# Kernel tuning notes

Hardware: AMD Instinct MI355X
Metric: run time of the kernel (lower is better)

The kernel has to match this reference:

```python
import jax, jax.numpy as jnp
import numpy as np

NEG_BIG = -9e15
ALPHA = 0.2  # LeakyReLU negative slope


def _gatm_layer(x, adj_mask, M, W, a_self, a_neighs):
    # x: [N, Fin], adj_mask: [N, N] bool, M: [N, N]
    h = x @ W                                   # [N, Fout]
    s = h @ a_self                              # [N, 1]
    n = h @ a_neighs                            # [N, 1]
    e = s + n.T                                 # [N, N] broadcast additive score
    e = jax.nn.leaky_relu(e * M, negative_slope=ALPHA)
    scores = jnp.where(adj_mask, e, NEG_BIG)
    attention = jax.nn.softmax(scores, axis=1)  # row-wise
    h_prime = attention @ h                     # [N, Fout]
    return jax.nn.elu(h_prime)                  # concat=True path


def setup_inputs() -> dict:
    key = jax.random.key(0)
    ks = jax.random.split(key, 8)
    N, D0, D1, D2 = 8192, 512, 256, 64
    scale = 0.05
    return {
        "x": jax.random.normal(ks[0], (N, D0), dtype=jnp.float32),
        "adj": jax.random.randint(ks[1], (N, N), 0, 2, dtype=jnp.int32),
        "M": jax.random.uniform(ks[2], (N, N), dtype=jnp.float32),
        "W0": jax.random.normal(ks[3], (D0, D1), dtype=jnp.float32) * scale,
        "a_self0": jax.random.normal(ks[4], (D1, 1), dtype=jnp.float32) * scale,
        "a_neighs0": jax.random.normal(ks[5], (D1, 1), dtype=jnp.float32) * scale,
        "W1": jax.random.normal(ks[6], (D1, D2), dtype=jnp.float32) * scale,
        "a_self1": jax.random.normal(ks[7], (D2, 1), dtype=jnp.float32) * scale,
        "a_neighs1": jax.random.normal(jax.random.fold_in(key, 99), (D2, 1), dtype=jnp.float32) * scale,
    }


def reference(x, adj, M, W0, a_self0, a_neighs0, W1, a_self1, a_neighs1):
    adj_mask = adj > 0
    x = _gatm_layer(x, adj_mask, M, W0, a_self0, a_neighs0)
    x = _gatm_layer(x, adj_mask, M, W1, a_self1, a_neighs1)
    return x
```

## Files before the change

kernel.cpp:

```cpp
#include <hip/hip_runtime.h>
#include <hip/hip_bf16.h>

constexpr int NN = 8192;
using uint = unsigned int;

typedef __bf16 bf16x8 __attribute__((ext_vector_type(8)));
typedef float f32x4 __attribute__((ext_vector_type(4)));
typedef float f32x16 __attribute__((ext_vector_type(16)));
typedef unsigned short ushort8_t __attribute__((ext_vector_type(8)));

__device__ __forceinline__ float eluf(float z) { return z > 0.f ? z : __expf(z) - 1.f; }

__device__ __forceinline__ unsigned short bf16_hi(float v) {
  unsigned u = __float_as_uint(v);
  unsigned r = u + 0x7fffu + ((u >> 16) & 1u);
  return (unsigned short)(r >> 16);
}
__device__ __forceinline__ float bf16_tof(unsigned short u) {
  return __uint_as_float(((unsigned)u) << 16);
}

__device__ __forceinline__ uint cvt_pk_bf16(float a, float b) {
  uint r;
  asm("v_cvt_pk_bf16_f32 %0, %1, %2" : "=v"(r) : "v"(a), "v"(b));
  return r;
}

__device__ __forceinline__ void lds_barrier() {
  asm volatile("s_waitcnt lgkmcnt(0)" ::: "memory");
  __builtin_amdgcn_s_barrier();
}

template<int K, int NOUT>
__global__ __launch_bounds__(256) void gemm_kernel(
    const float* __restrict__ A, const float* __restrict__ W, float* __restrict__ C) {
  constexpr int BM = 64, BN = 64, BK = 16;
  __shared__ __align__(16) float As[BK][BM + 4];
  __shared__ __align__(16) float Ws[BK][BN];
  const int t = threadIdx.x;
  const int i0 = blockIdx.x * BM;
  const int c0 = blockIdx.y * BN;
  const int tr = t >> 4;
  const int tc = t & 15;
  const int lr = t >> 2;
  const int lk = (t & 3) * 4;
  const int wk = t >> 4;
  const int wc = (t & 15) * 4;
  float acc[4][4] = {};
  for (int k0 = 0; k0 < K; k0 += BK) {
    const float4 a4 = *reinterpret_cast<const float4*>(&A[(size_t)(i0 + lr) * K + k0 + lk]);
    As[lk + 0][lr] = a4.x; As[lk + 1][lr] = a4.y;
    As[lk + 2][lr] = a4.z; As[lk + 3][lr] = a4.w;
    *reinterpret_cast<float4*>(&Ws[wk][wc]) =
        *reinterpret_cast<const float4*>(&W[(size_t)(k0 + wk) * NOUT + c0 + wc]);
    __syncthreads();
    #pragma unroll
    for (int kk = 0; kk < BK; ++kk) {
      const float4 av = *reinterpret_cast<const float4*>(&As[kk][4 * tr]);
      const float4 wv = *reinterpret_cast<const float4*>(&Ws[kk][4 * tc]);
      const float a[4] = {av.x, av.y, av.z, av.w};
      const float w[4] = {wv.x, wv.y, wv.z, wv.w};
      #pragma unroll
      for (int i = 0; i < 4; ++i)
        #pragma unroll
        for (int j = 0; j < 4; ++j) acc[i][j] += a[i] * w[j];
    }
    __syncthreads();
  }
  #pragma unroll
  for (int i = 0; i < 4; ++i) {
    const float4 o = make_float4(acc[i][0], acc[i][1], acc[i][2], acc[i][3]);
    *reinterpret_cast<float4*>(&C[(size_t)(i0 + 4 * tr + i) * NOUT + c0 + 4 * tc]) = o;
  }
}

__global__ __launch_bounds__(256) void splitx_kernel(
    const float* __restrict__ X, unsigned short* __restrict__ Th,
    unsigned short* __restrict__ Tl) {
  const size_t tid = (size_t)blockIdx.x * 256 + threadIdx.x;
  const int kt = (int)(tid >> 13);
  const int row = (int)(tid & 8191);
  const float* src = X + (size_t)row * 512 + kt * 32;
  #pragma unroll
  for (int kc = 0; kc < 4; ++kc) {
    ushort8_t hi, lo;
    #pragma unroll
    for (int e = 0; e < 8; ++e) {
      const float v = src[kc * 8 + e];
      const unsigned short h = bf16_hi(v);
      hi[e] = h;
      lo[e] = bf16_hi(v - bf16_tof(h));
    }
    const size_t o = ((size_t)(kt * 4 + kc) * 8192 + row) * 8;
    *reinterpret_cast<ushort8_t*>(&Th[o]) = hi;
    *reinterpret_cast<ushort8_t*>(&Tl[o]) = lo;
  }
}

__global__ __launch_bounds__(256) void splitw_kernel(
    const float* __restrict__ W, unsigned short* __restrict__ Th,
    unsigned short* __restrict__ Tl) {
  const int tid = blockIdx.x * 256 + threadIdx.x;
  const int kb = tid >> 8;
  const int col = tid & 255;
  ushort8_t hi, lo;
  #pragma unroll
  for (int e = 0; e < 8; ++e) {
    const float v = W[(size_t)(kb * 8 + e) * 256 + col];
    const unsigned short h = bf16_hi(v);
    hi[e] = h;
    lo[e] = bf16_hi(v - bf16_tof(h));
  }
  const size_t o = ((size_t)kb * 256 + col) * 8;
  *reinterpret_cast<ushort8_t*>(&Th[o]) = hi;
  *reinterpret_cast<ushort8_t*>(&Tl[o]) = lo;
}

__global__ __launch_bounds__(512) void gemm1_mfma_kernel(
    const unsigned short* __restrict__ Axh, const unsigned short* __restrict__ Axl,
    const unsigned short* __restrict__ Bwh, const unsigned short* __restrict__ Bwl,
    float* __restrict__ C) {
  const int t = threadIdx.x;
  const int lane = t & 63;
  const int cf = t >> 6;
  const int i0 = blockIdx.x * 32;
  const int col = cf * 32 + (lane & 31);
  const size_t abase = ((size_t)(lane >> 5) * 8192 + i0 + (lane & 31)) * 8;
  const size_t bbase = ((size_t)(lane >> 5) * 256 + col) * 8;

  f32x16 acc;
  #pragma unroll
  for (int i = 0; i < 16; ++i) acc[i] = 0.f;

  #pragma unroll 2
  for (int kt = 0; kt < 16; ++kt) {
    const size_t at = (size_t)kt * 4 * 8192 * 8;
    const size_t bt = (size_t)kt * 4 * 256 * 8;
    #pragma unroll
    for (int h = 0; h < 2; ++h) {
      const size_t ao = at + (size_t)h * 2 * 8192 * 8 + abase;
      const size_t bo = bt + (size_t)h * 2 * 256 * 8 + bbase;
      const bf16x8 ah = *reinterpret_cast<const bf16x8*>(Axh + ao);
      const bf16x8 al = *reinterpret_cast<const bf16x8*>(Axl + ao);
      const bf16x8 bh = *reinterpret_cast<const bf16x8*>(Bwh + bo);
      const bf16x8 bl = *reinterpret_cast<const bf16x8*>(Bwl + bo);
      acc = __builtin_amdgcn_mfma_f32_32x32x16_bf16(al, bh, acc, 0, 0, 0);
      acc = __builtin_amdgcn_mfma_f32_32x32x16_bf16(ah, bl, acc, 0, 0, 0);
      acc = __builtin_amdgcn_mfma_f32_32x32x16_bf16(ah, bh, acc, 0, 0, 0);
    }
  }

  #pragma unroll
  for (int reg = 0; reg < 16; ++reg) {
    const int row = (reg & 3) + 8 * (reg >> 2) + 4 * (lane >> 5);
    C[(size_t)(i0 + row) * 256 + col] = acc[reg];
  }
}

template<int FOUT>
__global__ __launch_bounds__(256) void sn_kernel(
    const float* __restrict__ H, const float* __restrict__ a_self,
    const float* __restrict__ a_neigh, float* __restrict__ s, float* __restrict__ n) {
  const int wave = threadIdx.x >> 6;
  const int lane = threadIdx.x & 63;
  const int row = blockIdx.x * 4 + wave;
  float ds = 0.f, dn = 0.f;
  #pragma unroll
  for (int c = lane; c < FOUT; c += 64) {
    const float h = H[(size_t)row * FOUT + c];
    ds += h * a_self[c];
    dn += h * a_neigh[c];
  }
  #pragma unroll
  for (int off = 32; off > 0; off >>= 1) {
    ds += __shfl_down(ds, off);
    dn += __shfl_down(dn, off);
  }
  if (lane == 0) { s[row] = ds; n[row] = dn; }
}

template<int F>
__global__ __launch_bounds__(256) void split_kernel(
    const float* __restrict__ H, unsigned short* __restrict__ Th,
    unsigned short* __restrict__ Tl) {
  const int t = threadIdx.x;
  const int tile = blockIdx.x;
  const int c = t & (F - 1);
  const int kcb = t / F;
  for (int kc = kcb; kc < 4; kc += 256 / F) {
    ushort8_t hi, lo;
    #pragma unroll
    for (int e = 0; e < 8; ++e) {
      float v = H[(size_t)(tile * 32 + kc * 8 + e) * F + c];
      unsigned short h = bf16_hi(v);
      hi[e] = h;
      lo[e] = bf16_hi(v - bf16_tof(h));
    }
    size_t o = ((size_t)(tile * 4 + kc) * F + c) * 8;
    *reinterpret_cast<ushort8_t*>(&Th[o]) = hi;
    *reinterpret_cast<ushort8_t*>(&Tl[o]) = lo;
  }
}

__global__ __launch_bounds__(256) void mask_kernel(
    const int* __restrict__ adj, uint* __restrict__ Bm) {
  const size_t tg = (size_t)blockIdx.x * 256 + threadIdx.x;
  const int4 a = *reinterpret_cast<const int4*>(&adj[tg * 4]);
  uint nib = (a.x > 0 ? 1u : 0u) | (a.y > 0 ? 2u : 0u) |
             (a.z > 0 ? 4u : 0u) | (a.w > 0 ? 8u : 0u);
  const int lane = threadIdx.x & 63;
  uint v = nib << ((lane & 7) * 4);
  v |= __shfl_xor(v, 1);
  v |= __shfl_xor(v, 2);
  v |= __shfl_xor(v, 4);
  if ((lane & 7) == 0) Bm[tg >> 3] = v;
}

template<int F>
__global__ __launch_bounds__(256) void combine_kernel(
    const float* __restrict__ pO, const float* __restrict__ pL, float* __restrict__ out) {
  const size_t q = (size_t)blockIdx.x * 256 + threadIdx.x;
  const size_t base = q * 4;
  const int row = (int)(base / F);
  const float4 a = *reinterpret_cast<const float4*>(pO + base);
  const float4 b = *reinterpret_cast<const float4*>(pO + (size_t)8192 * F + base);
  const float il = 1.0f / (pL[row] + pL[8192 + row]);
  float4 o;
  o.x = eluf((a.x + b.x) * il);
  o.y = eluf((a.y + b.y) * il);
  o.z = eluf((a.z + b.z) * il);
  o.w = eluf((a.w + b.w) * il);
  *reinterpret_cast<float4*>(out + base) = o;
}

__global__ __launch_bounds__(1024, 4) void attn1_kernel(
    const float* __restrict__ Mm, const uint* __restrict__ Bm,
    const float* __restrict__ sv, const float* __restrict__ nv,
    const unsigned short* __restrict__ Th, const unsigned short* __restrict__ Tl,
    float* __restrict__ pO, float* __restrict__ pL) {
  constexpr int F = 256, NT = 4096 / 64;
  __shared__ __align__(16) uint Pa[2][2][2][8 * 132];
  __shared__ __align__(16) float nvs[8192];
  __shared__ float l_lds[64];

  const int t = threadIdx.x;
  const int lane = t & 63;
  const int w = t >> 6;
  const int cf = w & 7;
  const int ks = w >> 3;
  const int r = t >> 5;
  const int p2 = t & 31;
  const int i0 = blockIdx.x * 64;
  const int jh = blockIdx.y;
  const size_t jbase = (size_t)jh * 4096;
  const int jt = jh * 128;

  reinterpret_cast<float4*>(nvs)[t] = reinterpret_cast<const float4*>(nv + jbase)[t];

  const float svrA = sv[i0 + r];
  const float svrB = sv[i0 + 32 + r];
  const size_t mrowA = (size_t)(i0 + r) * NN + jbase;
  const size_t mrowB = mrowA + (size_t)32 * NN;
  const uint* mkrowA = Bm + (size_t)(i0 + r) * (NN / 32) + jh * 128;
  const uint* mkrowB = mkrowA + (size_t)32 * (NN / 32);
  const int col = cf * 32 + (lane & 31);
  const size_t bo0 = ((size_t)(lane >> 5) * F + col) * 8;
  const int pidx = (p2 >> 2) * 132 + r * 4 + (p2 & 3);
  const int aidx = (ks * 4 + (lane >> 5)) * 132 + (lane & 31) * 4;

  float2 MA_e = *reinterpret_cast<const float2*>(&Mm[mrowA + 2 * p2]);
  float2 MA_o = *reinterpret_cast<const float2*>(&Mm[mrowA + 64 + 2 * p2]);
  float2 MB_e = *reinterpret_cast<const float2*>(&Mm[mrowB + 2 * p2]);
  float2 MB_o = *reinterpret_cast<const float2*>(&Mm[mrowB + 64 + 2 * p2]);
  uint mkA_e = mkrowA[p2 >> 4];
  uint mkA_o = mkrowA[2 + (p2 >> 4)];
  uint mkB_e = mkrowB[p2 >> 4];
  uint mkB_o = mkrowB[2 + (p2 >> 4)];
  const size_t tb0 = (size_t)(jt + ks) * 8192;
  bf16x8 bh0_e = *reinterpret_cast<const bf16x8*>(Th + tb0 + bo0);
  bf16x8 bl0_e = *reinterpret_cast<const bf16x8*>(Tl + tb0 + bo0);
  bf16x8 bh1_e = *reinterpret_cast<const bf16x8*>(Th + tb0 + bo0 + 4096);
  bf16x8 bl1_e = *reinterpret_cast<const bf16x8*>(Tl + tb0 + bo0 + 4096);
  bf16x8 bh0_o, bl0_o, bh1_o, bl1_o;

  float rsumA = 0.f, rsumB = 0.f;
  f32x16 accA, accB;
  #pragma unroll
  for (int i = 0; i < 16; ++i) { accA[i] = 0.f; accB[i] = 0.f; }

  __syncthreads();

  float2 nv_e = *reinterpret_cast<const float2*>(&nvs[2 * p2]);
  float2 nv_o = *reinterpret_cast<const float2*>(&nvs[64 + 2 * p2]);

#define STEP1(TJ, MCA, MKA, MCB, MKB, NVC, BH0C, BL0C, BH1C, BL1C, BH0N, BL0N, BH1N, BL1N) \
  {                                                                               \
    const int t_j = (TJ);                                                         \
    const int jb = (t_j + 1 < NT) ? t_j + 1 : 0;                                  \
    const size_t tb = (size_t)(jt + 2 * jb + ks) * 8192;                          \
    BH0N = *reinterpret_cast<const bf16x8*>(Th + tb + bo0);                       \
    BL0N = *reinterpret_cast<const bf16x8*>(Tl + tb + bo0);                       \
    BH1N = *reinterpret_cast<const bf16x8*>(Th + tb + bo0 + 4096);                \
    BL1N = *reinterpret_cast<const bf16x8*>(Tl + tb + bo0 + 4096);                \
    float e0 = (svrA + NVC.x) * MCA.x; e0 = fmaxf(e0, 0.2f * e0); e0 = fminf(e0, 70.f); \
    float e1 = (svrA + NVC.y) * MCA.y; e1 = fmaxf(e1, 0.2f * e1); e1 = fminf(e1, 70.f); \
    float e2 = (svrB + NVC.x) * MCB.x; e2 = fmaxf(e2, 0.2f * e2); e2 = fminf(e2, 70.f); \
    float e3 = (svrB + NVC.y) * MCB.y; e3 = fmaxf(e3, 0.2f * e3); e3 = fminf(e3, 70.f); \
    const float pA0 = ((MKA >> (2 * (p2 & 15))) & 1u) ? __expf(e0) : 0.f;         \
    const float pA1 = ((MKA >> (2 * (p2 & 15) + 1)) & 1u) ? __expf(e1) : 0.f;     \
    const float pB0 = ((MKB >> (2 * (p2 & 15))) & 1u) ? __expf(e2) : 0.f;         \
    const float pB1 = ((MKB >> (2 * (p2 & 15) + 1)) & 1u) ? __expf(e3) : 0.f;     \
    rsumA += pA0 + pA1; rsumB += pB0 + pB1;                                       \
    const int jm = (t_j + 2 < NT) ? t_j + 2 : 0;                                  \
    MCA = *reinterpret_cast<const float2*>(&Mm[mrowA + (size_t)jm * 64 + 2 * p2]); \
    MKA = mkrowA[jm * 2 + (p2 >> 4)];                                             \
    MCB = *reinterpret_cast<const float2*>(&Mm[mrowB + (size_t)jm * 64 + 2 * p2]); \
    MKB = mkrowB[jm * 2 + (p2 >> 4)];                                             \
    NVC = *reinterpret_cast<const float2*>(&nvs[jm * 64 + 2 * p2]);               \
    const uint hwA = cvt_pk_bf16(pA0, pA1);                                       \
    const uint lwA = cvt_pk_bf16(pA0 - __uint_as_float(hwA << 16),                \
                                 pA1 - __uint_as_float(hwA & 0xffff0000u));       \
    const uint hwB = cvt_pk_bf16(pB0, pB1);                                       \
    const uint lwB = cvt_pk_bf16(pB0 - __uint_as_float(hwB << 16),                \
                                 pB1 - __uint_as_float(hwB & 0xffff0000u));       \
    Pa[t_j & 1][0][0][pidx] = hwA;                                                \
    Pa[t_j & 1][1][0][pidx] = lwA;                                                \
    Pa[t_j & 1][0][1][pidx] = hwB;                                                \
    Pa[t_j & 1][1][1][pidx] = lwB;                                                \
    lds_barrier();                                                                \
    const bf16x8 ahA0 = *reinterpret_cast<const bf16x8*>(&Pa[t_j & 1][0][0][aidx]);       \
    const bf16x8 alA0 = *reinterpret_cast<const bf16x8*>(&Pa[t_j & 1][1][0][aidx]);       \
    const bf16x8 ahA1 = *reinterpret_cast<const bf16x8*>(&Pa[t_j & 1][0][0][aidx + 264]); \
    const bf16x8 alA1 = *reinterpret_cast<const bf16x8*>(&Pa[t_j & 1][1][0][aidx + 264]); \
    const bf16x8 ahB0 = *reinterpret_cast<const bf16x8*>(&Pa[t_j & 1][0][1][aidx]);       \
    const bf16x8 alB0 = *reinterpret_cast<const bf16x8*>(&Pa[t_j & 1][1][1][aidx]);       \
    const bf16x8 ahB1 = *reinterpret_cast<const bf16x8*>(&Pa[t_j & 1][0][1][aidx + 264]); \
    const bf16x8 alB1 = *reinterpret_cast<const bf16x8*>(&Pa[t_j & 1][1][1][aidx + 264]); \
    accA = __builtin_amdgcn_mfma_f32_32x32x16_bf16(alA0, BH0C, accA, 0, 0, 0);    \
    accB = __builtin_amdgcn_mfma_f32_32x32x16_bf16(alB0, BH0C, accB, 0, 0, 0);    \
    accA = __builtin_amdgcn_mfma_f32_32x32x16_bf16(ahA0, BL0C, accA, 0, 0, 0);    \
    accB = __builtin_amdgcn_mfma_f32_32x32x16_bf16(ahB0, BL0C, accB, 0, 0, 0);    \
    accA = __builtin_amdgcn_mfma_f32_32x32x16_bf16(ahA0, BH0C, accA, 0, 0, 0);    \
    accB = __builtin_amdgcn_mfma_f32_32x32x16_bf16(ahB0, BH0C, accB, 0, 0, 0);    \
    accA = __builtin_amdgcn_mfma_f32_32x32x16_bf16(alA1, BH1C, accA, 0, 0, 0);    \
    accB = __builtin_amdgcn_mfma_f32_32x32x16_bf16(alB1, BH1C, accB, 0, 0, 0);    \
    accA = __builtin_amdgcn_mfma_f32_32x32x16_bf16(ahA1, BL1C, accA, 0, 0, 0);    \
    accB = __builtin_amdgcn_mfma_f32_32x32x16_bf16(ahB1, BL1C, accB, 0, 0, 0);    \
    accA = __builtin_amdgcn_mfma_f32_32x32x16_bf16(ahA1, BH1C, accA, 0, 0, 0);    \
    accB = __builtin_amdgcn_mfma_f32_32x32x16_bf16(ahB1, BH1C, accB, 0, 0, 0);    \
  }

  for (int tj = 0; tj < NT; tj += 2) {
    STEP1(tj,     MA_e, mkA_e, MB_e, mkB_e, nv_e, bh0_e, bl0_e, bh1_e, bl1_e, bh0_o, bl0_o, bh1_o, bl1_o)
    STEP1(tj + 1, MA_o, mkA_o, MB_o, mkB_o, nv_o, bh0_o, bl0_o, bh1_o, bl1_o, bh0_e, bl0_e, bh1_e, bl1_e)
  }
#undef STEP1

  #pragma unroll
  for (int off = 1; off < 32; off <<= 1) {
    rsumA += __shfl_xor(rsumA, off);
    rsumB += __shfl_xor(rsumB, off);
  }
  if (p2 == 0) { l_lds[r] = rsumA; l_lds[32 + r] = rsumB; }
  __syncthreads();
  if (t < 64) pL[(size_t)jh * 8192 + i0 + t] = l_lds[t];

  float* scratch = nvs;
  if (ks == 1) {
    #pragma unroll
    for (int reg = 0; reg < 16; ++reg) scratch[cf * 1024 + reg * 64 + lane] = accA[reg];
  }
  __syncthreads();
  if (ks == 0) {
    #pragma unroll
    for (int reg = 0; reg < 16; ++reg) {
      const int row = (reg & 3) + 8 * (reg >> 2) + 4 * (lane >> 5);
      pO[(size_t)jh * 8192 * F + (size_t)(i0 + row) * F + col] =
          accA[reg] + scratch[cf * 1024 + reg * 64 + lane];
    }
  }
  __syncthreads();
  if (ks == 1) {
    #pragma unroll
    for (int reg = 0; reg < 16; ++reg) scratch[cf * 1024 + reg * 64 + lane] = accB[reg];
  }
  __syncthreads();
  if (ks == 0) {
    #pragma unroll
    for (int reg = 0; reg < 16; ++reg) {
      const int row = (reg & 3) + 8 * (reg >> 2) + 4 * (lane >> 5);
      pO[(size_t)jh * 8192 * F + (size_t)(i0 + 32 + row) * F + col] =
          accB[reg] + scratch[cf * 1024 + reg * 64 + lane];
    }
  }
}

__global__ __launch_bounds__(1024, 4) void attn2_kernel(
    const float* __restrict__ Mm, const uint* __restrict__ Bm,
    const float* __restrict__ sv, const float* __restrict__ nv,
    const unsigned short* __restrict__ Th, const unsigned short* __restrict__ Tl,
    float* __restrict__ pO, float* __restrict__ pL) {
  constexpr int F = 64, NT = 4096 / 64;
  __shared__ __align__(16) uint Pa[2][2][2][8 * 132];
  __shared__ __align__(16) float nvs[4096];
  __shared__ float l_lds[64];

  const int t = threadIdx.x;
  const int lane = t & 63;
  const int w = t >> 6;
  const int rb = w & 1;
  const int cf = (w >> 1) & 3;
  const int ks = w >> 3;
  const int r = t >> 5;
  const int p2 = t & 31;
  const int i0 = blockIdx.x * 64;
  const int jh = blockIdx.y;
  const size_t jbase = (size_t)jh * 4096;
  const int jt = jh * 128;

  reinterpret_cast<float4*>(nvs)[t] = reinterpret_cast<const float4*>(nv + jbase)[t];

  const float svrA = sv[i0 + r];
  const float svrB = sv[i0 + 32 + r];
  const size_t mrowA = (size_t)(i0 + r) * NN + jbase;
  const size_t mrowB = mrowA + (size_t)32 * NN;
  const uint* mkrowA = Bm + (size_t)(i0 + r) * (NN / 32) + jh * 128;
  const uint* mkrowB = mkrowA + (size_t)32 * (NN / 32);
  const int col = cf * 16 + (lane & 15);
  const size_t bo2 = ((size_t)(lane >> 4) * F + col) * 8;
  const int pidx = (p2 >> 2) * 132 + r * 4 + (p2 & 3);
  const int aidx = (ks * 4 + (lane >> 4)) * 132 + (rb * 16 + (lane & 15)) * 4;

  float2 MA_e = *reinterpret_cast<const float2*>(&Mm[mrowA + 2 * p2]);
  float2 MA_o = *reinterpret_cast<const float2*>(&Mm[mrowA + 64 + 2 * p2]);
  float2 MB_e = *reinterpret_cast<const float2*>(&Mm[mrowB + 2 * p2]);
  float2 MB_o = *reinterpret_cast<const float2*>(&Mm[mrowB + 64 + 2 * p2]);
  uint mkA_e = mkrowA[p2 >> 4];
  uint mkA_o = mkrowA[2 + (p2 >> 4)];
  uint mkB_e = mkrowB[p2 >> 4];
  uint mkB_o = mkrowB[2 + (p2 >> 4)];
  const size_t tb0 = (size_t)(jt + ks) * 2048;
  bf16x8 bh_e = *reinterpret_cast<const bf16x8*>(Th + tb0 + bo2);
  bf16x8 bl_e = *reinterpret_cast<const bf16x8*>(Tl + tb0 + bo2);
  bf16x8 bh_o, bl_o;

  float rsumA = 0.f, rsumB = 0.f;
  f32x4 accA = {0.f, 0.f, 0.f, 0.f}, accA2 = {0.f, 0.f, 0.f, 0.f};
  f32x4 accB = {0.f, 0.f, 0.f, 0.f}, accB2 = {0.f, 0.f, 0.f, 0.f};

  __syncthreads();

  float2 nv_e = *reinterpret_cast<const float2*>(&nvs[2 * p2]);
  float2 nv_o = *reinterpret_cast<const float2*>(&nvs[64 + 2 * p2]);

#define STEP2(TJ, MCA, MKA, MCB, MKB, NVC, BHC, BLC, BHN, BLN)                    \
  {                                                                               \
    const int t_j = (TJ);                                                         \
    const int jb = (t_j + 1 < NT) ? t_j + 1 : 0;                                  \
    const size_t tb = (size_t)(jt + 2 * jb + ks) * 2048;                          \
    BHN = *reinterpret_cast<const bf16x8*>(Th + tb + bo2);                        \
    BLN = *reinterpret_cast<const bf16x8*>(Tl + tb + bo2);                        \
    float e0 = (svrA + NVC.x) * MCA.x; e0 = fmaxf(e0, 0.2f * e0); e0 = fminf(e0, 70.f); \
    float e1 = (svrA + NVC.y) * MCA.y; e1 = fmaxf(e1, 0.2f * e1); e1 = fminf(e1, 70.f); \
    float e2 = (svrB + NVC.x) * MCB.x; e2 = fmaxf(e2, 0.2f * e2); e2 = fminf(e2, 70.f); \
    float e3 = (svrB + NVC.y) * MCB.y; e3 = fmaxf(e3, 0.2f * e3); e3 = fminf(e3, 70.f); \
    const float pA0 = ((MKA >> (2 * (p2 & 15))) & 1u) ? __expf(e0) : 0.f;         \
    const float pA1 = ((MKA >> (2 * (p2 & 15) + 1)) & 1u) ? __expf(e1) : 0.f;     \
    const float pB0 = ((MKB >> (2 * (p2 & 15))) & 1u) ? __expf(e2) : 0.f;         \
    const float pB1 = ((MKB >> (2 * (p2 & 15) + 1)) & 1u) ? __expf(e3) : 0.f;     \
    rsumA += pA0 + pA1; rsumB += pB0 + pB1;                                       \
    const int jm = (t_j + 2 < NT) ? t_j + 2 : 0;                                  \
    MCA = *reinterpret_cast<const float2*>(&Mm[mrowA + (size_t)jm * 64 + 2 * p2]); \
    MKA = mkrowA[jm * 2 + (p2 >> 4)];                                             \
    MCB = *reinterpret_cast<const float2*>(&Mm[mrowB + (size_t)jm * 64 + 2 * p2]); \
    MKB = mkrowB[jm * 2 + (p2 >> 4)];                                             \
    NVC = *reinterpret_cast<const float2*>(&nvs[jm * 64 + 2 * p2]);               \
    const uint hwA = cvt_pk_bf16(pA0, pA1);                                       \
    const uint lwA = cvt_pk_bf16(pA0 - __uint_as_float(hwA << 16),                \
                                 pA1 - __uint_as_float(hwA & 0xffff0000u));       \
    const uint hwB = cvt_pk_bf16(pB0, pB1);                                       \
    const uint lwB = cvt_pk_bf16(pB0 - __uint_as_float(hwB << 16),                \
                                 pB1 - __uint_as_float(hwB & 0xffff0000u));       \
    Pa[t_j & 1][0][0][pidx] = hwA;                                                \
    Pa[t_j & 1][1][0][pidx] = lwA;                                                \
    Pa[t_j & 1][0][1][pidx] = hwB;                                                \
    Pa[t_j & 1][1][1][pidx] = lwB;                                                \
    lds_barrier();                                                                \
    const bf16x8 ahA = *reinterpret_cast<const bf16x8*>(&Pa[t_j & 1][0][0][aidx]); \
    const bf16x8 alA = *reinterpret_cast<const bf16x8*>(&Pa[t_j & 1][1][0][aidx]); \
    const bf16x8 ahB = *reinterpret_cast<const bf16x8*>(&Pa[t_j & 1][0][1][aidx]); \
    const bf16x8 alB = *reinterpret_cast<const bf16x8*>(&Pa[t_j & 1][1][1][aidx]); \
    accA  = __builtin_amdgcn_mfma_f32_16x16x32_bf16(alA, BHC, accA, 0, 0, 0);     \
    accB  = __builtin_amdgcn_mfma_f32_16x16x32_bf16(alB, BHC, accB, 0, 0, 0);     \
    accA2 = __builtin_amdgcn_mfma_f32_16x16x32_bf16(ahA, BLC, accA2, 0, 0, 0);    \
    accB2 = __builtin_amdgcn_mfma_f32_16x16x32_bf16(ahB, BLC, accB2, 0, 0, 0);    \
    accA  = __builtin_amdgcn_mfma_f32_16x16x32_bf16(ahA, BHC, accA, 0, 0, 0);     \
    accB  = __builtin_amdgcn_mfma_f32_16x16x32_bf16(ahB, BHC, accB, 0, 0, 0);     \
  }

  for (int tj = 0; tj < NT; tj += 2) {
    STEP2(tj,     MA_e, mkA_e, MB_e, mkB_e, nv_e, bh_e, bl_e, bh_o, bl_o)
    STEP2(tj + 1, MA_o, mkA_o, MB_o, mkB_o, nv_o, bh_o, bl_o, bh_e, bl_e)
  }
#undef STEP2

  #pragma unroll
  for (int off = 1; off < 32; off <<= 1) {
    rsumA += __shfl_xor(rsumA, off);
    rsumB += __shfl_xor(rsumB, off);
  }
  if (p2 == 0) { l_lds[r] = rsumA; l_lds[32 + r] = rsumB; }
  __syncthreads();
  if (t < 64) pL[(size_t)jh * 8192 + i0 + t] = l_lds[t];

  float* scratch = nvs;
  if (ks == 1) {
    #pragma unroll
    for (int reg = 0; reg < 4; ++reg)
      scratch[(w & 7) * 256 + reg * 64 + lane] = accA[reg] + accA2[reg];
  }
  __syncthreads();
  if (ks == 0) {
    #pragma unroll
    for (int reg = 0; reg < 4; ++reg) {
      const int row = rb * 16 + (lane >> 4) * 4 + reg;
      pO[(size_t)jh * 8192 * F + (size_t)(i0 + row) * F + col] =
          accA[reg] + accA2[reg] + scratch[(w & 7) * 256 + reg * 64 + lane];
    }
  }
  __syncthreads();
  if (ks == 1) {
    #pragma unroll
    for (int reg = 0; reg < 4; ++reg)
      scratch[(w & 7) * 256 + reg * 64 + lane] = accB[reg] + accB2[reg];
  }
  __syncthreads();
  if (ks == 0) {
    #pragma unroll
    for (int reg = 0; reg < 4; ++reg) {
      const int row = rb * 16 + (lane >> 4) * 4 + reg;
      pO[(size_t)jh * 8192 * F + (size_t)(i0 + 32 + row) * F + col] =
          accB[reg] + accB2[reg] + scratch[(w & 7) * 256 + reg * 64 + lane];
    }
  }
}

extern "C" void kernel_launch(void* const* d_in, const int* in_sizes, int n_in,
                              void* d_out, int out_size, void* d_ws, size_t ws_size,
                              hipStream_t stream) {
  const float* x   = (const float*)d_in[0];
  const int*   adj = (const int*)  d_in[1];
  const float* Mm  = (const float*)d_in[2];
  const float* W0  = (const float*)d_in[3];
  const float* as0 = (const float*)d_in[4];
  const float* an0 = (const float*)d_in[5];
  const float* W1  = (const float*)d_in[6];
  const float* as1 = (const float*)d_in[7];
  const float* an1 = (const float*)d_in[8];
  float* out = (float*)d_out;

  char* ws = (char*)d_ws;
  const size_t MB = 1048576;
  const size_t KB = 1024;
  float* h0  = (float*)(ws);
  uint*  Bm  = (uint*) (ws);
  float* x1  = (float*)(ws + 8 * MB);
  float* h1  = (float*)(ws + 16 * MB);
  unsigned short* Th0 = (unsigned short*)(ws + 18 * MB);
  unsigned short* Tl0 = (unsigned short*)(ws + 22 * MB);
  unsigned short* Th1 = (unsigned short*)(ws + 26 * MB);
  unsigned short* Tl1 = (unsigned short*)(ws + 27 * MB);
  float* s0  = (float*)(ws + 28 * MB);
  float* n0  = (float*)(ws + 28 * MB + 32 * KB);
  float* s1  = (float*)(ws + 28 * MB + 64 * KB);
  float* n1  = (float*)(ws + 28 * MB + 96 * KB);
  float* pL1 = (float*)(ws + 28 * MB + 128 * KB);
  float* pL2 = (float*)(ws + 28 * MB + 192 * KB);
  float* pO1 = (float*)(ws + 29 * MB);
  float* pO2 = (float*)(ws + 29 * MB);
  unsigned short* Txh = (unsigned short*)(ws + 64 * MB);
  unsigned short* Txl = (unsigned short*)(ws + 72 * MB);
  unsigned short* Twh = (unsigned short*)(ws + 80 * MB);
  unsigned short* Twl = (unsigned short*)(ws + 81 * MB);

  splitx_kernel<<<dim3(512), dim3(256), 0, stream>>>(x, Txh, Txl);
  splitw_kernel<<<dim3(64), dim3(256), 0, stream>>>(W0, Twh, Twl);
  gemm1_mfma_kernel<<<dim3(256), dim3(512), 0, stream>>>(Txh, Txl, Twh, Twl, h0);
  sn_kernel<256><<<dim3(2048), dim3(256), 0, stream>>>(h0, as0, an0, s0, n0);
  split_kernel<256><<<dim3(256), dim3(256), 0, stream>>>(h0, Th0, Tl0);
  mask_kernel<<<dim3(65536), dim3(256), 0, stream>>>(adj, Bm);
  attn1_kernel<<<dim3(128, 2), dim3(1024), 0, stream>>>(Mm, Bm, s0, n0, Th0, Tl0, pO1, pL1);
  combine_kernel<256><<<dim3(2048), dim3(256), 0, stream>>>(pO1, pL1, x1);
  gemm_kernel<256, 64><<<dim3(128, 1), dim3(256), 0, stream>>>(x1, W1, h1);
  sn_kernel<64><<<dim3(2048), dim3(256), 0, stream>>>(h1, as1, an1, s1, n1);
  split_kernel<64><<<dim3(256), dim3(256), 0, stream>>>(h1, Th1, Tl1);
  attn2_kernel<<<dim3(128, 2), dim3(1024), 0, stream>>>(Mm, Bm, s1, n1, Th1, Tl1, pO2, pL2);
  combine_kernel<64><<<dim3(512), dim3(256), 0, stream>>>(pO2, pL2, out);
}
```

Measured before the change: 329.4 us.

## Fuse split into gemm1 epilogue and fuse combine+gemm2+sn+split for layer two

The bf16 hi/lo split of h0 now happens in the gemm1 epilogue, which removes the separate split kernel and its re-read of h0. For the second layer, the combine (normalize plus ELU) is folded into the A-tile load of the fp32 GEMM. The s/n dot products and the hi/lo split are computed in that GEMM's epilogue, which removes the x1 and h1 round trips and three launches. The costs are scattered 2-byte stores in both epilogues and an extra tiny kernel that computes the inverse row sums.

```diff
diff --git a/kernel.cpp b/kernel.cpp
--- a/kernel.cpp
+++ b/kernel.cpp
@@ -29,49 +29,6 @@
 __device__ __forceinline__ void lds_barrier() {
   asm volatile("s_waitcnt lgkmcnt(0)" ::: "memory");
   __builtin_amdgcn_s_barrier();
-}
-
-template<int K, int NOUT>
-__global__ __launch_bounds__(256) void gemm_kernel(
-    const float* __restrict__ A, const float* __restrict__ W, float* __restrict__ C) {
-  constexpr int BM = 64, BN = 64, BK = 16;
-  __shared__ __align__(16) float As[BK][BM + 4];
-  __shared__ __align__(16) float Ws[BK][BN];
-  const int t = threadIdx.x;
-  const int i0 = blockIdx.x * BM;
-  const int c0 = blockIdx.y * BN;
-  const int tr = t >> 4;
-  const int tc = t & 15;
-  const int lr = t >> 2;
-  const int lk = (t & 3) * 4;
-  const int wk = t >> 4;
-  const int wc = (t & 15) * 4;
-  float acc[4][4] = {};
-  for (int k0 = 0; k0 < K; k0 += BK) {
-    const float4 a4 = *reinterpret_cast<const float4*>(&A[(size_t)(i0 + lr) * K + k0 + lk]);
-    As[lk + 0][lr] = a4.x; As[lk + 1][lr] = a4.y;
-    As[lk + 2][lr] = a4.z; As[lk + 3][lr] = a4.w;
-    *reinterpret_cast<float4*>(&Ws[wk][wc]) =
-        *reinterpret_cast<const float4*>(&W[(size_t)(k0 + wk) * NOUT + c0 + wc]);
-    __syncthreads();
-    #pragma unroll
-    for (int kk = 0; kk < BK; ++kk) {
-      const float4 av = *reinterpret_cast<const float4*>(&As[kk][4 * tr]);
-      const float4 wv = *reinterpret_cast<const float4*>(&Ws[kk][4 * tc]);
-      const float a[4] = {av.x, av.y, av.z, av.w};
-      const float w[4] = {wv.x, wv.y, wv.z, wv.w};
-      #pragma unroll
-      for (int i = 0; i < 4; ++i)
-        #pragma unroll
-        for (int j = 0; j < 4; ++j) acc[i][j] += a[i] * w[j];
-    }
-    __syncthreads();
-  }
-  #pragma unroll
-  for (int i = 0; i < 4; ++i) {
-    const float4 o = make_float4(acc[i][0], acc[i][1], acc[i][2], acc[i][3]);
-    *reinterpret_cast<float4*>(&C[(size_t)(i0 + 4 * tr + i) * NOUT + c0 + 4 * tc]) = o;
-  }
 }
 
 __global__ __launch_bounds__(256) void splitx_kernel(
@@ -119,7 +76,8 @@
 __global__ __launch_bounds__(512) void gemm1_mfma_kernel(
     const unsigned short* __restrict__ Axh, const unsigned short* __restrict__ Axl,
     const unsigned short* __restrict__ Bwh, const unsigned short* __restrict__ Bwl,
-    float* __restrict__ C) {
+    float* __restrict__ C, unsigned short* __restrict__ Th,
+    unsigned short* __restrict__ Tl) {
   const int t = threadIdx.x;
   const int lane = t & 63;
   const int cf = t >> 6;
@@ -153,7 +111,13 @@
   #pragma unroll
   for (int reg = 0; reg < 16; ++reg) {
     const int row = (reg & 3) + 8 * (reg >> 2) + 4 * (lane >> 5);
-    C[(size_t)(i0 + row) * 256 + col] = acc[reg];
+    const float v = acc[reg];
+    C[(size_t)(i0 + row) * 256 + col] = v;
+    const unsigned short h = bf16_hi(v);
+    const unsigned short l = bf16_hi(v - bf16_tof(h));
+    const size_t o = ((size_t)(blockIdx.x * 4 + (row >> 3)) * 256 + col) * 8 + (row & 7);
+    Th[o] = h;
+    Tl[o] = l;
   }
 }
 
@@ -177,29 +141,6 @@
     dn += __shfl_down(dn, off);
   }
   if (lane == 0) { s[row] = ds; n[row] = dn; }
-}
-
-template<int F>
-__global__ __launch_bounds__(256) void split_kernel(
-    const float* __restrict__ H, unsigned short* __restrict__ Th,
-    unsigned short* __restrict__ Tl) {
-  const int t = threadIdx.x;
-  const int tile = blockIdx.x;
-  const int c = t & (F - 1);
-  const int kcb = t / F;
-  for (int kc = kcb; kc < 4; kc += 256 / F) {
-    ushort8_t hi, lo;
-    #pragma unroll
-    for (int e = 0; e < 8; ++e) {
-      float v = H[(size_t)(tile * 32 + kc * 8 + e) * F + c];
-      unsigned short h = bf16_hi(v);
-      hi[e] = h;
-      lo[e] = bf16_hi(v - bf16_tof(h));
-    }
-    size_t o = ((size_t)(tile * 4 + kc) * F + c) * 8;
-    *reinterpret_cast<ushort8_t*>(&Th[o]) = hi;
-    *reinterpret_cast<ushort8_t*>(&Tl[o]) = lo;
-  }
 }
 
 __global__ __launch_bounds__(256) void mask_kernel(
@@ -214,6 +155,12 @@
   v |= __shfl_xor(v, 2);
   v |= __shfl_xor(v, 4);
   if ((lane & 7) == 0) Bm[tg >> 3] = v;
+}
+
+__global__ __launch_bounds__(256) void plsum_kernel(
+    const float* __restrict__ pL, float* __restrict__ il) {
+  const int i = blockIdx.x * 256 + threadIdx.x;
+  il[i] = 1.0f / (pL[i] + pL[8192 + i]);
 }
 
 template<int F>
@@ -231,6 +178,93 @@
   o.z = eluf((a.z + b.z) * il);
   o.w = eluf((a.w + b.w) * il);
   *reinterpret_cast<float4*>(out + base) = o;
+}
+
+__global__ __launch_bounds__(256) void gemm2_fused_kernel(
+    const float* __restrict__ pO1, const float* __restrict__ il1,
+    const float* __restrict__ W, const float* __restrict__ a_self,
+    const float* __restrict__ a_neigh, unsigned short* __restrict__ Th,
+    unsigned short* __restrict__ Tl, float* __restrict__ s1,
+    float* __restrict__ n1) {
+  constexpr int K = 256, NOUT = 64, BM = 64, BK = 16;
+  const size_t seg = (size_t)8192 * 256;
+  __shared__ __align__(16) float As[BK][BM + 4];
+  __shared__ __align__(16) float Ws[BK][NOUT];
+  __shared__ float red_s[64][17];
+  __shared__ float red_n[64][17];
+  const int t = threadIdx.x;
+  const int i0 = blockIdx.x * BM;
+  const int tr = t >> 4;
+  const int tc = t & 15;
+  const int lr = t >> 2;
+  const int lk = (t & 3) * 4;
+  const int wk = t >> 4;
+  const int wc = (t & 15) * 4;
+  const float ilr = il1[i0 + lr];
+  float acc[4][4] = {};
+  for (int k0 = 0; k0 < K; k0 += BK) {
+    const size_t aoff = (size_t)(i0 + lr) * 256 + k0 + lk;
+    const float4 p0 = *reinterpret_cast<const float4*>(&pO1[aoff]);
+    const float4 p1 = *reinterpret_cast<const float4*>(&pO1[seg + aoff]);
+    As[lk + 0][lr] = eluf((p0.x + p1.x) * ilr);
+    As[lk + 1][lr] = eluf((p0.y + p1.y) * ilr);
+    As[lk + 2][lr] = eluf((p0.z + p1.z) * ilr);
+    As[lk + 3][lr] = eluf((p0.w + p1.w) * ilr);
+    *reinterpret_cast<float4*>(&Ws[wk][wc]) =
+        *reinterpret_cast<const float4*>(&W[(size_t)(k0 + wk) * NOUT + wc]);
+    __syncthreads();
+    #pragma unroll
+    for (int kk = 0; kk < BK; ++kk) {
+      const float4 av = *reinterpret_cast<const float4*>(&As[kk][4 * tr]);
+      const float4 wv = *reinterpret_cast<const float4*>(&Ws[kk][4 * tc]);
+      const float a[4] = {av.x, av.y, av.z, av.w};
+      const float w[4] = {wv.x, wv.y, wv.z, wv.w};
+      #pragma unroll
+      for (int i = 0; i < 4; ++i)
+        #pragma unroll
+        for (int j = 0; j < 4; ++j) acc[i][j] += a[i] * w[j];
+    }
+    __syncthreads();
+  }
+  float asv[4], anv[4];
+  #pragma unroll
+  for (int j = 0; j < 4; ++j) {
+    asv[j] = a_self[4 * tc + j];
+    anv[j] = a_neigh[4 * tc + j];
+  }
+  #pragma unroll
+  for (int i = 0; i < 4; ++i) {
+    float ps = 0.f, pn = 0.f;
+    #pragma unroll
+    for (int j = 0; j < 4; ++j) { ps += acc[i][j] * asv[j]; pn += acc[i][j] * anv[j]; }
+    red_s[4 * tr + i][tc] = ps;
+    red_n[4 * tr + i][tc] = pn;
+  }
+  #pragma unroll
+  for (int i = 0; i < 4; ++i) {
+    const int row = 4 * tr + i;
+    const int tile = 2 * blockIdx.x + (row >> 5);
+    const int kc = (row >> 3) & 3;
+    const int e = row & 7;
+    #pragma unroll
+    for (int j = 0; j < 4; ++j) {
+      const int col = 4 * tc + j;
+      const float v = acc[i][j];
+      const unsigned short h = bf16_hi(v);
+      const unsigned short l = bf16_hi(v - bf16_tof(h));
+      const size_t o = ((size_t)(tile * 4 + kc) * 64 + col) * 8 + e;
+      Th[o] = h;
+      Tl[o] = l;
+    }
+  }
+  __syncthreads();
+  if (t < 64) {
+    float ss = 0.f, nn = 0.f;
+    #pragma unroll
+    for (int q = 0; q < 16; ++q) { ss += red_s[t][q]; nn += red_n[t][q]; }
+    s1[i0 + t] = ss;
+    n1[i0 + t] = nn;
+  }
 }
 
 __global__ __launch_bounds__(1024, 4) void attn1_kernel(
@@ -564,8 +598,6 @@
   const size_t KB = 1024;
   float* h0  = (float*)(ws);
   uint*  Bm  = (uint*) (ws);
-  float* x1  = (float*)(ws + 8 * MB);
-  float* h1  = (float*)(ws + 16 * MB);
   unsigned short* Th0 = (unsigned short*)(ws + 18 * MB);
   unsigned short* Tl0 = (unsigned short*)(ws + 22 * MB);
   unsigned short* Th1 = (unsigned short*)(ws + 26 * MB);
@@ -576,6 +608,7 @@
   float* n1  = (float*)(ws + 28 * MB + 96 * KB);
   float* pL1 = (float*)(ws + 28 * MB + 128 * KB);
   float* pL2 = (float*)(ws + 28 * MB + 192 * KB);
+  float* il1 = (float*)(ws + 28 * MB + 256 * KB);
   float* pO1 = (float*)(ws + 29 * MB);
   float* pO2 = (float*)(ws + 29 * MB);
   unsigned short* Txh = (unsigned short*)(ws + 64 * MB);
@@ -585,15 +618,13 @@
 
   splitx_kernel<<<dim3(512), dim3(256), 0, stream>>>(x, Txh, Txl);
   splitw_kernel<<<dim3(64), dim3(256), 0, stream>>>(W0, Twh, Twl);
-  gemm1_mfma_kernel<<<dim3(256), dim3(512), 0, stream>>>(Txh, Txl, Twh, Twl, h0);
+  gemm1_mfma_kernel<<<dim3(256), dim3(512), 0, stream>>>(Txh, Txl, Twh, Twl, h0, Th0, Tl0);
   sn_kernel<256><<<dim3(2048), dim3(256), 0, stream>>>(h0, as0, an0, s0, n0);
-  split_kernel<256><<<dim3(256), dim3(256), 0, stream>>>(h0, Th0, Tl0);
   mask_kernel<<<dim3(65536), dim3(256), 0, stream>>>(adj, Bm);
   attn1_kernel<<<dim3(128, 2), dim3(1024), 0, stream>>>(Mm, Bm, s0, n0, Th0, Tl0, pO1, pL1);
-  combine_kernel<256><<<dim3(2048), dim3(256), 0, stream>>>(pO1, pL1, x1);
-  gemm_kernel<256, 64><<<dim3(128, 1), dim3(256), 0, stream>>>(x1, W1, h1);
-  sn_kernel<64><<<dim3(2048), dim3(256), 0, stream>>>(h1, as1, an1, s1, n1);
-  split_kernel<64><<<dim3(256), dim3(256), 0, stream>>>(h1, Th1, Tl1);
+  plsum_kernel<<<dim3(32), dim3(256), 0, stream>>>(pL1, il1);
+  gemm2_fused_kernel<<<dim3(128), dim3(256), 0, stream>>>(pO1, il1, W1, as1, an1,
+                                                          Th1, Tl1, s1, n1);
   attn2_kernel<<<dim3(128, 2), dim3(1024), 0, stream>>>(Mm, Bm, s1, n1, Th1, Tl1, pO2, pL2);
   combine_kernel<64><<<dim3(512), dim3(256), 0, stream>>>(pO2, pL2, out);
 }
```

After: 325.0 us. About the same (-1.3%).
